# Performance work log

Measured on AMD Instinct MI355X. Metric: run time of the kernel, lower is better.

Reference implementation:

```python
import jax, jax.numpy as jnp
import numpy as np

B, C, D, J = 8, 2048, 128, 128

def setup_inputs() -> dict:
    key = jax.random.key(0)
    ks = jax.random.split(key, 24)
    s = 0.02
    inp = {
        "operation_features": jax.random.normal(ks[0], (B, C, D), jnp.float32),
        "relations": jax.random.randint(ks[1], (B, C - 2, 2), 0, C, jnp.int64),
        "begins_idx": jax.random.randint(ks[2], (B, J), 0, C, jnp.int64),
        "ends_idx": jax.random.randint(ks[3], (B, J), 0, C, jnp.int64),
        "same_type_mask": (jax.random.uniform(ks[4], (B, C, C)) > 0.5).astype(jnp.float32),
        # BeginEndEncoder
        "W_begin": jax.random.normal(ks[5], (D, D), jnp.float32) * s,
        "b_begin": jnp.zeros((D,), jnp.float32),
        "W_end": jax.random.normal(ks[6], (D, D), jnp.float32) * s,
        "b_end": jnp.zeros((D,), jnp.float32),
        # OperationTimeRelationEncoder.mix: Linear(3D -> D)
        "W_mix3": jax.random.normal(ks[7], (3 * D, D), jnp.float32) * s,
        "b_mix3": jnp.zeros((D,), jnp.float32),
        # SelfAttention (hidden_dim = D)
        "W_qkv": jax.random.normal(ks[8], (D, 3 * D), jnp.float32) * s,
        "b_qkv": jnp.zeros((3 * D,), jnp.float32),
        "w_score": jax.random.normal(ks[9], (2 * D,), jnp.float32) * s,
        "b_score": jnp.zeros((), jnp.float32),
        "W_out": jax.random.normal(ks[10], (D, D), jnp.float32) * s,
        "b_out": jnp.zeros((D,), jnp.float32),
        # block mix: Linear(2D -> D)
        "W_mix2": jax.random.normal(ks[11], (2 * D, D), jnp.float32) * s,
        "b_mix2": jnp.zeros((D,), jnp.float32),
    }
    return inp

def _gather_ops(ops, idx):
    # ops: [B,C,D], idx: [B,M] -> [B,M,D]  (torch.gather along dim 1 with expanded index)
    Bb, _, Dd = ops.shape
    M = idx.shape[1]
    return jnp.take_along_axis(ops, jnp.broadcast_to(idx[:, :, None], (Bb, M, Dd)), axis=1)

def reference(operation_features, relations, begins_idx, ends_idx, same_type_mask,
              W_begin, b_begin, W_end, b_end, W_mix3, b_mix3,
              W_qkv, b_qkv, w_score, b_score, W_out, b_out, W_mix2, b_mix2):
    ops = operation_features
    Dd = ops.shape[-1]
    # --- OperationTimeRelationEncoder ---
    pred = _gather_ops(ops, relations[..., 0])      # [B,C-2,D]
    succ = _gather_ops(ops, relations[..., 1])      # [B,C-2,D]
    concated = jnp.concatenate([ops[:, :-2, :], pred, succ], axis=-1)  # [B,C-2,3D]
    mixed = concated @ W_mix3 + b_mix3              # [B,C-2,D]
    begin_f = _gather_ops(ops, begins_idx) @ W_begin + b_begin  # [B,J,D]
    end_f = _gather_ops(ops, ends_idx) @ W_end + b_end
    begin = jnp.mean(begin_f, axis=1)               # [B,D]
    end = jnp.mean(end_f, axis=1)
    seq = jnp.concatenate([mixed, begin[:, None, :], end[:, None, :]], axis=1)  # [B,C,D]
    # --- SelfAttention (GAT-style additive score, decomposed to avoid CxCx2h blowup) ---
    qkv = ops @ W_qkv + b_qkv                       # [B,C,3D]
    q, k, v = jnp.split(qkv, 3, axis=-1)
    sq = q @ w_score[:Dd]                           # [B,C]  q_i . w_q
    sk = k @ w_score[Dd:]                           # [B,C]  k_j . w_k
    scores = jax.nn.leaky_relu(sq[:, :, None] + sk[:, None, :] + b_score)  # [B,C,C]
    attn = jax.nn.softmax(scores * same_type_mask, axis=-1)                # multiplicative mask, as in torch
    weighted = jnp.einsum('bij,bjd->bid', attn, v)  # [B,C,D]
    same_type = weighted @ W_out + b_out            # [B,C,D]
    # --- final mix ---
    return jnp.concatenate([seq, same_type], axis=-1) @ W_mix2 + b_mix2  # [B,C,D]
```

## Files before the change

### kernel.cpp

```cpp
#include <hip/hip_runtime.h>
#include <cstddef>

typedef __bf16 bf16;
typedef __bf16 bf16x4 __attribute__((ext_vector_type(4)));
typedef __bf16 bf16x8 __attribute__((ext_vector_type(8)));
typedef float  f32x4  __attribute__((ext_vector_type(4)));

#define MFMA16(a, b, c) __builtin_amdgcn_mfma_f32_16x16x32_bf16((a), (b), (c), 0, 0, 0)

#define BB 8
#define CC 2048
#define DD 128
#define JJN 128

#define WS_PK    ((size_t)0)
#define WS_OATT  ((size_t)4194304)
#define WS_OPS16 ((size_t)8388608)
#define WS_SQF   ((size_t)12582912)
#define WS_SKF   ((size_t)12648448)
#define WS_G1T   ((size_t)12713984)
#define WS_G2T   ((size_t)12746752)
#define WS_G3T   ((size_t)12779520)
#define WS_WCT   ((size_t)12812288)
#define WS_GBT   ((size_t)12845056)
#define WS_GET   ((size_t)12877824)
#define WS_UQK   ((size_t)12910592)
#define WS_BBM   ((size_t)12911104)
#define WS_BBB   ((size_t)12911616)
#define WS_BBE   ((size_t)12912128)
#define WS_SC    ((size_t)12912640)

__global__ __launch_bounds__(256) void k_prepcast(
    const float* __restrict__ ops, bf16* __restrict__ ops16,
    const float* __restrict__ Wmix3, const float* __restrict__ Wmix2,
    const float* __restrict__ Wout,  const float* __restrict__ Wbegin,
    const float* __restrict__ Wend,  const float* __restrict__ Wqkv,
    const float* __restrict__ bqkv,  const float* __restrict__ wscore,
    const float* __restrict__ bscore,const float* __restrict__ bmix3,
    const float* __restrict__ bout,  const float* __restrict__ bmix2,
    const float* __restrict__ bbegin,const float* __restrict__ bend,
    bf16* __restrict__ G1T, bf16* __restrict__ G2T, bf16* __restrict__ G3T,
    bf16* __restrict__ WCT, bf16* __restrict__ GBT, bf16* __restrict__ GET,
    bf16* __restrict__ uqk, float* __restrict__ BBM, float* __restrict__ BBB,
    float* __restrict__ BBE, float* __restrict__ sc)
{
    __shared__ bf16  LshT[128 * 132];
    __shared__ float Rsh[128 * 8];
    int wg = blockIdx.x;
    int t  = threadIdx.x;

    if (wg < 1024) {
        size_t i = (size_t)wg * 256 + t;
        f32x4 a = *(const f32x4*)(ops + i * 8);
        f32x4 b = *(const f32x4*)(ops + i * 8 + 4);
        bf16x8 o;
        #pragma unroll
        for (int e = 0; e < 4; ++e) { o[e] = (bf16)a[e]; o[4 + e] = (bf16)b[e]; }
        *(bf16x8*)(ops16 + i * 8) = o;
        return;
    }
    if (wg < 1120) {
        int id  = wg - 1024;
        int mat = id >> 4, sub = id & 15;
        const float* L; const float* R; bf16* O;
        switch (mat) {
            case 0: L = Wmix3;           R = Wmix2;           O = G1T; break;
            case 1: L = Wmix3 + 128*128; R = Wmix2;           O = G2T; break;
            case 2: L = Wmix3 + 256*128; R = Wmix2;           O = G3T; break;
            case 3: L = Wout;            R = Wmix2 + 128*128; O = WCT; break;
            case 4: L = Wbegin;          R = Wmix2;           O = GBT; break;
            default:L = Wend;            R = Wmix2;           O = GET; break;
        }
        int e0 = sub * 8;
        #pragma unroll
        for (int pass = 0; pass < 16; ++pass) {
            int idx = pass * 256 + t;
            int d   = idx >> 5;
            int f0  = (idx & 31) * 4;
            f32x4 v = *(const f32x4*)(L + d * 128 + f0);
            #pragma unroll
            for (int jj = 0; jj < 4; ++jj)
                LshT[(f0 + jj) * 132 + d] = (bf16)v[jj];
        }
        #pragma unroll
        for (int pass = 0; pass < 4; ++pass) {
            int idx = pass * 256 + t;
            int f   = idx >> 3;
            int ee  = idx & 7;
            Rsh[f * 8 + ee] = R[f * 128 + e0 + ee];
        }
        __syncthreads();
        int ee = t >> 5;
        int e  = e0 + ee;
        int d0 = (t & 31) * 4;
        float s[4] = {0.f, 0.f, 0.f, 0.f};
        for (int f = 0; f < 128; ++f) {
            bf16x4 lv = *(const bf16x4*)&LshT[f * 132 + d0];
            float rv = Rsh[f * 8 + ee];
            #pragma unroll
            for (int dd = 0; dd < 4; ++dd)
                s[dd] += (float)lv[dd] * rv;
        }
        #pragma unroll
        for (int dd = 0; dd < 4; ++dd)
            O[e * 128 + d0 + dd] = (bf16)s[dd];
        return;
    }
    if (t < 128) {
        int d = t;
        float su = 0.f, sk_ = 0.f;
        for (int e2 = 0; e2 < 128; ++e2) {
            su  += Wqkv[d*384 + e2]       * wscore[e2];
            sk_ += Wqkv[d*384 + 128 + e2] * wscore[128 + e2];
        }
        uqk[d]       = (bf16)su;
        uqk[128 + d] = (bf16)sk_;
        int e = d;
        float bm = 0.f, bon = 0.f, bb_ = 0.f, be_ = 0.f;
        for (int f = 0; f < 128; ++f) {
            float w2a = Wmix2[f*128 + e];
            float w2b = Wmix2[(128+f)*128 + e];
            bm  += bmix3[f]  * w2a;
            bon += bout[f]   * w2b;
            bb_ += bbegin[f] * w2a;
            be_ += bend[f]   * w2a;
        }
        float bm2 = bmix2[e];
        BBM[e] = bm  + bon + bm2;
        BBB[e] = bb_ + bon + bm2;
        BBE[e] = be_ + bon + bm2;
    } else if (t == 128) {
        float cq = 0.f, ck = 0.f;
        for (int e2 = 0; e2 < 128; ++e2) {
            cq += bqkv[e2]       * wscore[e2];
            ck += bqkv[128 + e2] * wscore[128 + e2];
        }
        sc[0] = cq + bscore[0];
        sc[1] = ck;
    }
}

__global__ __launch_bounds__(256) void k_v(
    const bf16* __restrict__ ops16, const float* __restrict__ Wqkv,
    const float* __restrict__ bqkv, const bf16* __restrict__ uqk,
    const float* __restrict__ sc,
    bf16* __restrict__ PK, float* __restrict__ sqf, float* __restrict__ skf)
{
    __shared__ bf16 A[144 * 136];
    int b  = blockIdx.x >> 4;
    int jt = (blockIdx.x & 15) * 128;
    int t  = threadIdx.x;
    #pragma unroll
    for (int pass = 0; pass < 16; ++pass) {
        int idx = pass * 256 + t;
        int d   = idx >> 5;
        int n0  = (idx & 31) * 4;
        f32x4 v = *(const f32x4*)(Wqkv + d*384 + 256 + n0);
        #pragma unroll
        for (int jj = 0; jj < 4; ++jj)
            A[(n0 + jj)*136 + d] = (bf16)v[jj];
    }
    {
        int row = t >> 7, col = t & 127;
        A[(128 + row)*136 + col] = uqk[row*128 + col];
    }
    for (int idx = t; idx < 14*136; idx += 256)
        A[130*136 + idx] = (bf16)0.f;
    __syncthreads();

    int lane = t & 63, w = t >> 6;
    int m = lane & 15, q = lane >> 4;
    f32x4 acc[9][2];
    #pragma unroll
    for (int rb = 0; rb < 9; ++rb)
        #pragma unroll
        for (int cb = 0; cb < 2; ++cb)
            acc[rb][cb] = {0.f, 0.f, 0.f, 0.f};

    const bf16* opsb = ops16 + (size_t)b * CC * DD;
    #pragma unroll
    for (int kc = 0; kc < 4; ++kc) {
        bf16x8 bfr[2];
        #pragma unroll
        for (int cb = 0; cb < 2; ++cb) {
            int j = jt + w*32 + cb*16 + m;
            bfr[cb] = *(const bf16x8*)(opsb + (size_t)j*DD + kc*32 + q*8);
        }
        #pragma unroll
        for (int rb = 0; rb < 9; ++rb) {
            bf16x8 afr = *(const bf16x8*)&A[(rb*16 + m)*136 + kc*32 + q*8];
            acc[rb][0] = MFMA16(afr, bfr[0], acc[rb][0]);
            acc[rb][1] = MFMA16(afr, bfr[1], acc[rb][1]);
        }
    }
    float cqb = sc[0], ckv = sc[1];
    #pragma unroll
    for (int cb = 0; cb < 2; ++cb) {
        int j = jt + w*32 + cb*16 + m;
        if (q == 0) {
            sqf[b*CC + j] = acc[8][cb][0] + cqb;
            skf[b*CC + j] = acc[8][cb][1] + ckv;
        }
    }
    __syncthreads();
    bf16* pack = A;
    #pragma unroll
    for (int cb = 0; cb < 2; ++cb) {
        int qq_base = cb*2 + (m>>3);
        int e       = m & 7;
        #pragma unroll
        for (int rb = 0; rb < 8; ++rb) {
            #pragma unroll
            for (int r = 0; r < 4; ++r) {
                float v = acc[rb][cb][r] + bqkv[256 + rb*16 + q*4 + r];
                pack[w*4096 + rb*512 + qq_base*128 + (q*4+r)*8 + e] = (bf16)v;
            }
        }
    }
    __syncthreads();
    bf16* pkb = PK + (size_t)b * DD * CC + (size_t)jt * 128;
    #pragma unroll
    for (int pass = 0; pass < 8; ++pass) {
        int lidx = pass * 256 + t;
        *(uint4*)(pkb + (size_t)lidx * 8) = *(const uint4*)&pack[lidx * 8];
    }
}

struct MaskLd { f32x4 v[4]; };

__device__ __forceinline__ MaskLd stage_load(const float* __restrict__ mrow0,
                                             int st, int lane)
{
    MaskLd L;
    int rr0 = lane >> 4, cc = (lane & 15) * 4;
    const float* src = mrow0 + st * 64 + cc;
    #pragma unroll
    for (int k = 0; k < 4; ++k)
        L.v[k] = __builtin_nontemporal_load(
            (const f32x4*)(src + ((size_t)(rr0 + k * 4)) * CC));
    return L;
}

__device__ __forceinline__ void stage_write(const MaskLd& L, bf16* mb,
                                            int buf, int lane)
{
    int rr0 = lane >> 4, cc = (lane & 15) * 4;
    bf16* dst = mb + buf * 1152;
    #pragma unroll
    for (int k = 0; k < 4; ++k) {
        bf16x4 o;
        #pragma unroll
        for (int e = 0; e < 4; ++e) o[e] = (bf16)L.v[k][e];
        *(bf16x4*)(dst + (rr0 + k * 4) * 72 + cc) = o;
    }
}

__device__ __forceinline__ void load_vb(const bf16* __restrict__ pkb, int jc,
                                        int q, int m, bf16x8 vb[8])
{
    #pragma unroll
    for (int nb = 0; nb < 8; ++nb)
        vb[nb] = *(const bf16x8*)(pkb + ((size_t)(((jc*8 + nb)*4 + q)*16 + m)) * 8);
}

__device__ __forceinline__ void substep(const bf16* mb, const float* skb,
    int buf, int st, int sub, int q, int m, float sq, const bf16x8 vb[8],
    float& lsum, f32x4 acc[8])
{
    bf16x8 mk = *(const bf16x8*)(mb + buf * 1152 + m * 72 + sub * 32 + q * 8);
    int jo = st * 64 + sub * 32 + q * 8;
    f32x4 s0 = *(const f32x4*)(skb + jo);
    f32x4 s1 = *(const f32x4*)(skb + jo + 4);
    float sks[8] = {s0[0], s0[1], s0[2], s0[3], s1[0], s1[1], s1[2], s1[3]};
    bf16x8 a;
    #pragma unroll
    for (int e = 0; e < 8; ++e) {
        float tv = sq + sks[e];
        float lr = fmaxf(tv, 0.01f * tv);
        float z  = lr * (float)mk[e];
        float p  = __expf(z);
        lsum += p;
        a[e] = (bf16)p;
    }
    #pragma unroll
    for (int nb = 0; nb < 8; ++nb)
        acc[nb] = MFMA16(a, vb[nb], acc[nb]);
}

__global__ __launch_bounds__(256) void k_att(
    const float* __restrict__ mask, const bf16* __restrict__ PK,
    const float* __restrict__ sqf, const float* __restrict__ skf,
    bf16* __restrict__ Oatt)
{
    __shared__ __align__(16) char smem[35840];
    int t    = threadIdx.x;
    int lane = t & 63, w = t >> 6;
    int b    = blockIdx.x & 7;
    int i0   = (blockIdx.x >> 3) << 4;
    int m = lane & 15, q = lane >> 4;

    bf16*  mbuf = (bf16*)(smem + w * 6912);
    float* skb  = (float*)(smem + 27648 + w * 2048);

    {
        const float* src = skf + b*CC + w*512;
        f32x4 v0 = *(const f32x4*)(src + lane*4);
        f32x4 v1 = *(const f32x4*)(src + 256 + lane*4);
        *(f32x4*)(skb + lane*4) = v0;
        *(f32x4*)(skb + 256 + lane*4) = v1;
    }
    float sq = sqf[b*CC + i0 + m];
    const float* mrow0 = mask + ((size_t)(b*CC + i0))*CC + w*512;
    const bf16*  pkb   = PK + (size_t)b * DD * CC;
    int jc0 = w * 16;

    f32x4 acc[8];
    #pragma unroll
    for (int nb = 0; nb < 8; ++nb) acc[nb] = {0.f, 0.f, 0.f, 0.f};
    float lsum = 0.f;

    {   MaskLd r0 = stage_load(mrow0, 0, lane);
        stage_write(r0, mbuf, 0, lane); }
    MaskLd r1 = stage_load(mrow0, 1, lane);
    MaskLd r2 = stage_load(mrow0, 2, lane);
    MaskLd r3;
    bf16x8 vbA[8], vbB[8];
    load_vb(pkb, jc0, q, m, vbA);

    int bm = 0;
    for (int st = 0; st < 8; ++st) {
        if (st + 3 < 8) r3 = stage_load(mrow0, st + 3, lane);
        load_vb(pkb, jc0 + st*2 + 1, q, m, vbB);
        substep(mbuf, skb, bm, st, 0, q, m, sq, vbA, lsum, acc);
        if (st < 7) load_vb(pkb, jc0 + st*2 + 2, q, m, vbA);
        substep(mbuf, skb, bm, st, 1, q, m, sq, vbB, lsum, acc);
        int bw = bm + 1; if (bw == 3) bw = 0;
        if (st + 1 < 8) stage_write(r1, mbuf, bw, lane);
        r1 = r2; r2 = r3;
        bm = bw;
    }

    __syncthreads();
    float* Osh = (float*)smem;
    float* Lsh = (float*)(smem + 33792);
    lsum += __shfl_xor(lsum, 16, 64);
    lsum += __shfl_xor(lsum, 32, 64);
    if (q == 0) Lsh[w*16 + m] = lsum;
    #pragma unroll
    for (int nb = 0; nb < 8; ++nb)
        #pragma unroll
        for (int r = 0; r < 4; ++r)
            Osh[(w*16 + q*4 + r)*132 + nb*16 + m] = acc[nb][r];
    __syncthreads();

    int r  = t >> 4;
    int c0 = (t & 15) * 8;
    float l = Lsh[r] + Lsh[16 + r] + Lsh[32 + r] + Lsh[48 + r];
    float inv = 1.0f / l;
    bf16x8 o;
    #pragma unroll
    for (int e = 0; e < 8; ++e) {
        float s = Osh[r*132 + c0 + e] + Osh[(16 + r)*132 + c0 + e]
                + Osh[(32 + r)*132 + c0 + e] + Osh[(48 + r)*132 + c0 + e];
        o[e] = (bf16)(s * inv);
    }
    *(bf16x8*)(Oatt + ((size_t)(b*CC) + i0 + r)*DD + c0) = o;
}

__global__ __launch_bounds__(256) void k_epi(
    const bf16* __restrict__ ops16, const int* __restrict__ relations,
    const int* __restrict__ begins, const int* __restrict__ ends,
    const bf16* __restrict__ Oatt,
    const bf16* __restrict__ G1T, const bf16* __restrict__ G2T,
    const bf16* __restrict__ G3T, const bf16* __restrict__ WCT,
    const bf16* __restrict__ GBT, const bf16* __restrict__ GET,
    const float* __restrict__ BBM, const float* __restrict__ BBB,
    const float* __restrict__ BBE, float* __restrict__ out)
{
    __shared__ bf16 Abuf[32 * 136];
    __shared__ bf16 Bbuf[128 * 136];
    int t  = threadIdx.x;

    if (blockIdx.x >= 512) {
        __shared__ float meanv[2][128];
        int eidx  = (blockIdx.x - 512) * 2 + (t >> 7);
        int b     = eidx >> 1, which = eidx & 1;
        int tl    = t & 127;
        const int* idx = which ? (ends + b*JJN) : (begins + b*JJN);
        const bf16* opsb = ops16 + (size_t)b * CC * DD;
        float s = 0.f;
        for (int j = 0; j < JJN; ++j) {
            int rr = idx[j];
            s += (float)opsb[(size_t)rr*DD + tl];
        }
        meanv[t >> 7][tl] = s * (1.0f / (float)JJN);
        __syncthreads();
        const bf16* G   = which ? GET : GBT;
        const float* Bv = which ? BBE : BBB;
        const bf16* orow = Oatt + ((size_t)b*CC + (CC - 2 + which)) * DD;
        float a = Bv[tl];
        const bf16* gr = G + tl*128;
        const bf16* wr = WCT + tl*128;
        const float* mv = meanv[t >> 7];
        for (int d = 0; d < 128; ++d) {
            a += mv[d] * (float)gr[d];
            a += (float)orow[d] * (float)wr[d];
        }
        out[((size_t)b*CC + (CC - 2 + which))*DD + tl] = a;
        return;
    }

    int b  = blockIdx.x >> 6;
    int c0 = (blockIdx.x & 63) * 32;
    int lane = t & 63, w = t >> 6;
    int m = lane & 15, q = lane >> 4;

    f32x4 acc[2][2];
    #pragma unroll
    for (int rb = 0; rb < 2; ++rb)
        #pragma unroll
        for (int cb = 0; cb < 2; ++cb)
            acc[rb][cb] = {0.f, 0.f, 0.f, 0.f};

    const bf16* Bsrc[4] = {G1T, G2T, G3T, WCT};
    int arow = t >> 3, ao = (t & 7) * 16;
    int brow = t >> 1, bo = (t & 1) * 64;
    int c = c0 + arow;

    for (int term = 0; term < 4; ++term) {
        const bf16* src;
        if (term == 0)      src = ops16 + ((size_t)(b*CC + c)) * DD;
        else if (term == 3) src = Oatt  + ((size_t)(b*CC + c)) * DD;
        else {
            int ridx = relations[((size_t)b*(CC-2) + min(c, CC-3))*2 + (term - 1)];
            src = ops16 + ((size_t)(b*CC) + ridx) * DD;
        }
        *(uint4*)&Abuf[arow*136 + ao]     = *(const uint4*)(src + ao);
        *(uint4*)&Abuf[arow*136 + ao + 8] = *(const uint4*)(src + ao + 8);

        const uint4* bs = (const uint4*)(Bsrc[term] + brow*128 + bo);
        uint4* bd = (uint4*)&Bbuf[brow*136 + bo];
        #pragma unroll
        for (int ii = 0; ii < 8; ++ii) bd[ii] = bs[ii];
        __syncthreads();

        #pragma unroll
        for (int kc = 0; kc < 4; ++kc) {
            bf16x8 bfr[2];
            #pragma unroll
            for (int cb = 0; cb < 2; ++cb)
                bfr[cb] = *(const bf16x8*)&Bbuf[(w*32 + cb*16 + m)*136 + kc*32 + q*8];
            #pragma unroll
            for (int rb = 0; rb < 2; ++rb) {
                bf16x8 afr = *(const bf16x8*)&Abuf[(rb*16 + m)*136 + kc*32 + q*8];
                acc[rb][0] = MFMA16(afr, bfr[0], acc[rb][0]);
                acc[rb][1] = MFMA16(afr, bfr[1], acc[rb][1]);
            }
        }
        __syncthreads();
    }
    #pragma unroll
    for (int cb = 0; cb < 2; ++cb) {
        int col = w*32 + cb*16 + m;
        float bias = BBM[col];
        #pragma unroll
        for (int rb = 0; rb < 2; ++rb) {
            #pragma unroll
            for (int r = 0; r < 4; ++r) {
                int cg = c0 + rb*16 + q*4 + r;
                if (cg < CC - 2)
                    out[((size_t)(b*CC) + cg)*DD + col] = acc[rb][cb][r] + bias;
            }
        }
    }
}

extern "C" void kernel_launch(void* const* d_in, const int* in_sizes, int n_in,
                              void* d_out, int out_size, void* d_ws, size_t ws_size,
                              hipStream_t stream)
{
    const float* ops      = (const float*)d_in[0];
    const int*  relations = (const int*)d_in[1];
    const int*  begins    = (const int*)d_in[2];
    const int*  ends      = (const int*)d_in[3];
    const float* mask     = (const float*)d_in[4];
    const float* Wbegin   = (const float*)d_in[5];
    const float* bbegin   = (const float*)d_in[6];
    const float* Wend     = (const float*)d_in[7];
    const float* bend     = (const float*)d_in[8];
    const float* Wmix3    = (const float*)d_in[9];
    const float* bmix3    = (const float*)d_in[10];
    const float* Wqkv     = (const float*)d_in[11];
    const float* bqkv     = (const float*)d_in[12];
    const float* wscore   = (const float*)d_in[13];
    const float* bscore   = (const float*)d_in[14];
    const float* Wout     = (const float*)d_in[15];
    const float* bout     = (const float*)d_in[16];
    const float* Wmix2    = (const float*)d_in[17];
    const float* bmix2    = (const float*)d_in[18];
    float* outp = (float*)d_out;

    char* ws = (char*)d_ws;
    bf16*  PK    = (bf16*)(ws + WS_PK);
    bf16*  Oatt  = (bf16*)(ws + WS_OATT);
    bf16*  OPS16 = (bf16*)(ws + WS_OPS16);
    float* sqf   = (float*)(ws + WS_SQF);
    float* skf   = (float*)(ws + WS_SKF);
    bf16*  G1T   = (bf16*)(ws + WS_G1T);
    bf16*  G2T   = (bf16*)(ws + WS_G2T);
    bf16*  G3T   = (bf16*)(ws + WS_G3T);
    bf16*  WCT   = (bf16*)(ws + WS_WCT);
    bf16*  GBT   = (bf16*)(ws + WS_GBT);
    bf16*  GET   = (bf16*)(ws + WS_GET);
    bf16*  UQK   = (bf16*)(ws + WS_UQK);
    float* BBM   = (float*)(ws + WS_BBM);
    float* BBB   = (float*)(ws + WS_BBB);
    float* BBE   = (float*)(ws + WS_BBE);
    float* SC    = (float*)(ws + WS_SC);

    k_prepcast<<<dim3(1121), dim3(256), 0, stream>>>(
        ops, OPS16,
        Wmix3, Wmix2, Wout, Wbegin, Wend, Wqkv, bqkv, wscore, bscore,
        bmix3, bout, bmix2, bbegin, bend,
        G1T, G2T, G3T, WCT, GBT, GET, UQK, BBM, BBB, BBE, SC);

    k_v<<<dim3(128), dim3(256), 0, stream>>>(
        OPS16, Wqkv, bqkv, UQK, SC, PK, sqf, skf);

    k_att<<<dim3(1024), dim3(256), 0, stream>>>(
        mask, PK, sqf, skf, Oatt);

    k_epi<<<dim3(520), dim3(256), 0, stream>>>(
        OPS16, relations, begins, ends, Oatt,
        G1T, G2T, G3T, WCT, GBT, GET, BBM, BBB, BBE, outp);
}
```

Measured before the change: 296.2 us.

## Process two 16-row query tiles per attention block to reuse V loads

The attention kernel now handles 32 query rows per block (two 16-row tiles) and launches half as many blocks. Each V fragment loaded from global memory feeds MFMAs for both tiles, which halves V traffic per output row. The mask pipeline changes from a three-stage to a two-stage buffer with wider stages and padded rows. In exchange the kernel uses more LDS and registers (two accumulator sets, larger mask staging), so occupancy drops and less mask prefetch is in flight.

```diff
diff --git a/kernel.cpp b/kernel.cpp
--- a/kernel.cpp
+++ b/kernel.cpp
@@ -226,7 +226,7 @@
     }
 }
 
-struct MaskLd { f32x4 v[4]; };
+struct MaskLd { f32x4 v[8]; };
 
 __device__ __forceinline__ MaskLd stage_load(const float* __restrict__ mrow0,
                                              int st, int lane)
@@ -235,7 +235,7 @@
     int rr0 = lane >> 4, cc = (lane & 15) * 4;
     const float* src = mrow0 + st * 64 + cc;
     #pragma unroll
-    for (int k = 0; k < 4; ++k)
+    for (int k = 0; k < 8; ++k)
         L.v[k] = __builtin_nontemporal_load(
             (const f32x4*)(src + ((size_t)(rr0 + k * 4)) * CC));
     return L;
@@ -245,13 +245,13 @@
                                             int buf, int lane)
 {
     int rr0 = lane >> 4, cc = (lane & 15) * 4;
-    bf16* dst = mb + buf * 1152;
-    #pragma unroll
-    for (int k = 0; k < 4; ++k) {
+    bf16* dst = mb + buf * 2816;
+    #pragma unroll
+    for (int k = 0; k < 8; ++k) {
         bf16x4 o;
         #pragma unroll
         for (int e = 0; e < 4; ++e) o[e] = (bf16)L.v[k][e];
-        *(bf16x4*)(dst + (rr0 + k * 4) * 72 + cc) = o;
+        *(bf16x4*)(dst + (rr0 + k * 4) * 88 + cc) = o;
     }
 }
 
@@ -264,10 +264,11 @@
 }
 
 __device__ __forceinline__ void substep(const bf16* mb, const float* skb,
-    int buf, int st, int sub, int q, int m, float sq, const bf16x8 vb[8],
-    float& lsum, f32x4 acc[8])
-{
-    bf16x8 mk = *(const bf16x8*)(mb + buf * 1152 + m * 72 + sub * 32 + q * 8);
+    int buf, int st, int sub, int tile, int q, int m, float sq,
+    const bf16x8 vb[8], float& lsum, f32x4 acc[8])
+{
+    bf16x8 mk = *(const bf16x8*)(mb + buf * 2816 + (tile*16 + m) * 88
+                                 + sub * 32 + q * 8);
     int jo = st * 64 + sub * 32 + q * 8;
     f32x4 s0 = *(const f32x4*)(skb + jo);
     f32x4 s1 = *(const f32x4*)(skb + jo + 4);
@@ -292,15 +293,15 @@
     const float* __restrict__ sqf, const float* __restrict__ skf,
     bf16* __restrict__ Oatt)
 {
-    __shared__ __align__(16) char smem[35840];
+    __shared__ __align__(16) char smem[53248];
     int t    = threadIdx.x;
     int lane = t & 63, w = t >> 6;
     int b    = blockIdx.x & 7;
-    int i0   = (blockIdx.x >> 3) << 4;
+    int i0   = (blockIdx.x >> 3) << 5;
     int m = lane & 15, q = lane >> 4;
 
-    bf16*  mbuf = (bf16*)(smem + w * 6912);
-    float* skb  = (float*)(smem + 27648 + w * 2048);
+    bf16*  mbuf = (bf16*)(smem + w * 11264);
+    float* skb  = (float*)(smem + 45056 + w * 2048);
 
     {
         const float* src = skf + b*CC + w*512;
@@ -309,62 +310,71 @@
         *(f32x4*)(skb + lane*4) = v0;
         *(f32x4*)(skb + 256 + lane*4) = v1;
     }
-    float sq = sqf[b*CC + i0 + m];
+    float sq0 = sqf[b*CC + i0 + m];
+    float sq1 = sqf[b*CC + i0 + 16 + m];
     const float* mrow0 = mask + ((size_t)(b*CC + i0))*CC + w*512;
     const bf16*  pkb   = PK + (size_t)b * DD * CC;
     int jc0 = w * 16;
 
-    f32x4 acc[8];
-    #pragma unroll
-    for (int nb = 0; nb < 8; ++nb) acc[nb] = {0.f, 0.f, 0.f, 0.f};
-    float lsum = 0.f;
+    f32x4 acc0[8], acc1[8];
+    #pragma unroll
+    for (int nb = 0; nb < 8; ++nb) {
+        acc0[nb] = {0.f, 0.f, 0.f, 0.f};
+        acc1[nb] = {0.f, 0.f, 0.f, 0.f};
+    }
+    float lsum0 = 0.f, lsum1 = 0.f;
 
     {   MaskLd r0 = stage_load(mrow0, 0, lane);
         stage_write(r0, mbuf, 0, lane); }
     MaskLd r1 = stage_load(mrow0, 1, lane);
     MaskLd r2 = stage_load(mrow0, 2, lane);
-    MaskLd r3;
-    bf16x8 vbA[8], vbB[8];
-    load_vb(pkb, jc0, q, m, vbA);
-
-    int bm = 0;
+
+    int buf = 0;
     for (int st = 0; st < 8; ++st) {
-        if (st + 3 < 8) r3 = stage_load(mrow0, st + 3, lane);
-        load_vb(pkb, jc0 + st*2 + 1, q, m, vbB);
-        substep(mbuf, skb, bm, st, 0, q, m, sq, vbA, lsum, acc);
-        if (st < 7) load_vb(pkb, jc0 + st*2 + 2, q, m, vbA);
-        substep(mbuf, skb, bm, st, 1, q, m, sq, vbB, lsum, acc);
-        int bw = bm + 1; if (bw == 3) bw = 0;
-        if (st + 1 < 8) stage_write(r1, mbuf, bw, lane);
-        r1 = r2; r2 = r3;
-        bm = bw;
+        #pragma unroll
+        for (int sub = 0; sub < 2; ++sub) {
+            bf16x8 vb[8];
+            load_vb(pkb, jc0 + st*2 + sub, q, m, vb);
+            substep(mbuf, skb, buf, st, sub, 0, q, m, sq0, vb, lsum0, acc0);
+            substep(mbuf, skb, buf, st, sub, 1, q, m, sq1, vb, lsum1, acc1);
+        }
+        if (st + 1 < 8) stage_write(r1, mbuf, buf ^ 1, lane);
+        r1 = r2;
+        if (st + 3 < 8) r2 = stage_load(mrow0, st + 3, lane);
+        buf ^= 1;
     }
 
     __syncthreads();
     float* Osh = (float*)smem;
     float* Lsh = (float*)(smem + 33792);
-    lsum += __shfl_xor(lsum, 16, 64);
-    lsum += __shfl_xor(lsum, 32, 64);
-    if (q == 0) Lsh[w*16 + m] = lsum;
-    #pragma unroll
-    for (int nb = 0; nb < 8; ++nb)
-        #pragma unroll
-        for (int r = 0; r < 4; ++r)
-            Osh[(w*16 + q*4 + r)*132 + nb*16 + m] = acc[nb][r];
-    __syncthreads();
-
-    int r  = t >> 4;
-    int c0 = (t & 15) * 8;
-    float l = Lsh[r] + Lsh[16 + r] + Lsh[32 + r] + Lsh[48 + r];
-    float inv = 1.0f / l;
-    bf16x8 o;
-    #pragma unroll
-    for (int e = 0; e < 8; ++e) {
-        float s = Osh[r*132 + c0 + e] + Osh[(16 + r)*132 + c0 + e]
-                + Osh[(32 + r)*132 + c0 + e] + Osh[(48 + r)*132 + c0 + e];
-        o[e] = (bf16)(s * inv);
-    }
-    *(bf16x8*)(Oatt + ((size_t)(b*CC) + i0 + r)*DD + c0) = o;
+    #pragma unroll
+    for (int tile = 0; tile < 2; ++tile) {
+        float ls = tile ? lsum1 : lsum0;
+        ls += __shfl_xor(ls, 16, 64);
+        ls += __shfl_xor(ls, 32, 64);
+        if (q == 0) Lsh[w*16 + m] = ls;
+        const f32x4* acc = tile ? acc1 : acc0;
+        #pragma unroll
+        for (int nb = 0; nb < 8; ++nb)
+            #pragma unroll
+            for (int r = 0; r < 4; ++r)
+                Osh[(w*16 + q*4 + r)*132 + nb*16 + m] = acc[nb][r];
+        __syncthreads();
+
+        int r  = t >> 4;
+        int c0 = (t & 15) * 8;
+        float l = Lsh[r] + Lsh[16 + r] + Lsh[32 + r] + Lsh[48 + r];
+        float inv = 1.0f / l;
+        bf16x8 o;
+        #pragma unroll
+        for (int e = 0; e < 8; ++e) {
+            float s = Osh[r*132 + c0 + e] + Osh[(16 + r)*132 + c0 + e]
+                    + Osh[(32 + r)*132 + c0 + e] + Osh[(48 + r)*132 + c0 + e];
+            o[e] = (bf16)(s * inv);
+        }
+        *(bf16x8*)(Oatt + ((size_t)(b*CC) + i0 + tile*16 + r)*DD + c0) = o;
+        if (tile == 0) __syncthreads();
+    }
 }
 
 __global__ __launch_bounds__(256) void k_epi(
@@ -527,7 +537,7 @@
     k_v<<<dim3(128), dim3(256), 0, stream>>>(
         OPS16, Wqkv, bqkv, UQK, SC, PK, sqf, skf);
 
-    k_att<<<dim3(1024), dim3(256), 0, stream>>>(
+    k_att<<<dim3(512), dim3(256), 0, stream>>>(
         mask, PK, sqf, skf, Oatt);
 
     k_epi<<<dim3(520), dim3(256), 0, stream>>>(
```

After: 295.1 us. About the same (-0.4%).
